# Performance work log

Hardware: AMD Instinct MI355X
Metric: run time of the kernel (lower is better)

## Reference

```python
import jax, jax.numpy as jnp
import numpy as np

B, Q, K, G, M = 16, 2048, 1024, 512, 4096
PC_MIN = np.array([-75.2, -75.2, -2.0], np.float32)
PC_MAX = np.array([75.2, 75.2, 4.0], np.float32)
MAX_SIZE = np.array([20.0, 20.0, 8.0], np.float32)


def decode_boxes(b):
    # normalized (cx,cy,cz,l,w,h,rad) in [0,1] -> metric (x,y,z,dx,dy,dz,heading)
    xyz = b[:, :3] * jnp.asarray(PC_MAX - PC_MIN) + jnp.asarray(PC_MIN)
    lwh = b[:, 3:6] * jnp.asarray(MAX_SIZE) + 0.05
    rad = b[:, 6:7] * (2.0 * np.pi) - np.pi
    return jnp.concatenate([xyz, lwh, rad], -1)


def box_cxcyczlwh_to_xyxyxy(b):
    c, s = b[:, :3], b[:, 3:6]
    return jnp.concatenate([c - 0.5 * s, c + 0.5 * s], -1)


def generalized_box3d_iou(b1, b2):
    # full pairwise axis-aligned 3D GIoU, as in the original module
    vol1 = jnp.prod(b1[:, 3:] - b1[:, :3], -1)
    vol2 = jnp.prod(b2[:, 3:] - b2[:, :3], -1)
    lt = jnp.maximum(b1[:, None, :3], b2[None, :, :3])
    rb = jnp.minimum(b1[:, None, 3:], b2[None, :, 3:])
    inter = jnp.prod(jnp.clip(rb - lt, 0.0), -1)
    union = vol1[:, None] + vol2[None, :] - inter
    iou = inter / jnp.clip(union, 1e-7)
    ltc = jnp.minimum(b1[:, None, :3], b2[None, :, :3])
    rbc = jnp.maximum(b1[:, None, 3:], b2[None, :, 3:])
    volc = jnp.prod(jnp.clip(rbc - ltc, 0.0), -1)
    return iou - (volc - union) / jnp.clip(volc, 1e-7)


def _bev_corners(b):
    c, s = jnp.cos(b[:, 6]), jnp.sin(b[:, 6])
    hx, hy = b[:, 3] * 0.5, b[:, 4] * 0.5
    lx = jnp.stack([hx, hx, -hx, -hx], -1)  # (N,4)
    ly = jnp.stack([hy, -hy, -hy, hy], -1)
    gx = b[:, 0:1] + lx * c[:, None] - ly * s[:, None]
    gy = b[:, 1:2] + lx * s[:, None] + ly * c[:, None]
    return jnp.stack([gx, gy], -1)  # (N,4,2)


def _points_in_box(pts, b):  # pts (N,P,2)
    c, s = jnp.cos(b[:, 6:7]), jnp.sin(b[:, 6:7])
    dx = pts[..., 0] - b[:, 0:1]
    dy = pts[..., 1] - b[:, 1:2]
    qx = dx * c + dy * s
    qy = -dx * s + dy * c
    return (jnp.abs(qx) <= b[:, 3:4] * 0.5 + 1e-5) & (jnp.abs(qy) <= b[:, 4:5] * 0.5 + 1e-5)


def _cross(a, b):
    return a[..., 0] * b[..., 1] - a[..., 1] * b[..., 0]


def paired_boxes_iou3d(bA, bB):
    # paired rotated 3D IoU (OpenPCDet paired_boxes_iou3d_gpu semantics)
    N = bA.shape[0]
    ca, cb = _bev_corners(bA), _bev_corners(bB)
    a0, a1 = ca, jnp.roll(ca, -1, axis=1)
    e0, e1 = cb, jnp.roll(cb, -1, axis=1)
    da = (a1 - a0)[:, :, None, :]
    db = (e1 - e0)[:, None, :, :]
    dp = e0[:, None, :, :] - a0[:, :, None, :]
    den = _cross(da, db)  # (N,4,4)
    den_s = jnp.where(jnp.abs(den) > 1e-8, den, 1.0)
    t = _cross(dp, db) / den_s
    u = _cross(dp, da) / den_s
    ok = (jnp.abs(den) > 1e-8) & (t >= 0.0) & (t <= 1.0) & (u >= 0.0) & (u <= 1.0)
    ipts = a0[:, :, None, :] + t[..., None] * da  # (N,4,4,2)
    pts = jnp.concatenate([ca, cb, ipts.reshape(N, 16, 2)], 1)  # (N,24,2)
    mask = jnp.concatenate([_points_in_box(ca, bB), _points_in_box(cb, bA), ok.reshape(N, 16)], 1)
    w = mask.astype(pts.dtype)
    cnt = w.sum(-1)
    cen = (pts * w[..., None]).sum(1) / jnp.maximum(cnt, 1.0)[:, None]
    ang = jnp.arctan2(pts[..., 1] - cen[:, None, 1], pts[..., 0] - cen[:, None, 0])
    ang = jnp.where(mask, ang, 1e9)
    order = jnp.argsort(ang, axis=1)
    pts_s = jnp.take_along_axis(pts, order[..., None], 1)
    mask_s = jnp.take_along_axis(mask, order, 1)
    p0 = pts_s[:, 0]
    poly = jnp.where(mask_s[..., None], pts_s, p0[:, None, :])
    x, y = poly[..., 0], poly[..., 1]
    xn, yn = jnp.roll(x, -1, 1), jnp.roll(y, -1, 1)
    area = 0.5 * jnp.abs(jnp.sum(x * yn - xn * y, 1))
    inter_bev = jnp.where(cnt >= 3.0, area, 0.0)
    z_lo = jnp.maximum(bA[:, 2] - bA[:, 5] * 0.5, bB[:, 2] - bB[:, 5] * 0.5)
    z_hi = jnp.minimum(bA[:, 2] + bA[:, 5] * 0.5, bB[:, 2] + bB[:, 5] * 0.5)
    inter = inter_bev * jnp.clip(z_hi - z_lo, 0.0)
    v1 = jnp.prod(bA[:, 3:6], -1)
    v2 = jnp.prod(bB[:, 3:6], -1)
    return inter / jnp.clip(v1 + v2 - inter, 1e-7)


def setup_inputs() -> dict:
    key = jax.random.key(0)
    ks = jax.random.split(key, 6)
    pred_boxes = jax.random.uniform(ks[0], (B, Q, 7), jnp.float32)
    pred_ious = jax.random.uniform(ks[1], (B, Q, 1), jnp.float32)
    gt_boxes = jax.random.uniform(ks[2], (B, G, 7), jnp.float32)
    topk_indexes = jax.random.randint(ks[3], (B, K, 1), 0, Q)
    batch_idx = jnp.repeat(jnp.arange(B), M // B)
    src_idx = jax.random.randint(ks[4], (M,), 0, K)
    tgt_idx = jax.random.randint(ks[5], (M,), 0, G)
    return {"pred_boxes": pred_boxes, "pred_ious": pred_ious, "gt_boxes": gt_boxes,
            "topk_indexes": topk_indexes, "batch_idx": batch_idx, "src_idx": src_idx,
            "tgt_idx": tgt_idx, "num_boxes": M}


def reference(pred_boxes, pred_ious, gt_boxes, topk_indexes, batch_idx, src_idx, tgt_idx, num_boxes):
    Bn = pred_boxes.shape[0]
    topk = topk_indexes[..., 0]                       # (B,K)
    brange = jnp.arange(Bn)[:, None]
    pb = pred_boxes[brange, topk]                     # (B,K,7) gather
    pi = pred_ious[brange, topk]                      # (B,K,1)
    mp = pb[batch_idx, src_idx]                       # (M,7) matched preds
    mt = gt_boxes[batch_idx, tgt_idx]                 # (M,7) matched targets
    src_boxes, src_rads = mp[:, :6], mp[:, 6:]
    tgt_boxes, tgt_rads = mt[:, :6], mt[:, 6:]
    loss_bbox = jnp.abs(src_boxes - tgt_boxes).sum()
    loss_rad = jnp.abs(src_rads - tgt_rads).sum()
    giou = generalized_box3d_iou(box_cxcyczlwh_to_xyxyxy(src_boxes), box_cxcyczlwh_to_xyxyxy(tgt_boxes))
    gt_iou = jnp.diagonal(giou)                       # only the diagonal of the MxM matrix is used
    loss_giou = (1.0 - gt_iou).sum()
    pim = pi[batch_idx, src_idx]                      # (M,1)
    iou_t = paired_boxes_iou3d(decode_boxes(mp), decode_boxes(mt)) * 2.0 - 1.0
    iou_t = jax.lax.stop_gradient(iou_t)              # .detach() in original
    loss_iou = jnp.abs(pim - iou_t[:, None]).sum()
    nb = jnp.asarray(num_boxes, pred_boxes.dtype)
    # order: [loss_bbox, loss_giou, loss_rad, loss_iou]
    return jnp.stack([loss_bbox, loss_giou, loss_rad, loss_iou]) / nb
```

## Files before the change

kernel.cpp:

```cpp
#include <hip/hip_runtime.h>

#define B_ 16
#define Q_ 2048
#define K_ 1024
#define G_ 512
#define M_ 4096

__device__ __forceinline__ float bsum32(float v) {
#pragma unroll
  for (int o = 1; o < 32; o <<= 1) v += __shfl_xor(v, o, 64);
  return v;
}

__device__ __forceinline__ void corner_xy(float cx, float cy, float hx, float hy,
                                          float c, float s, int idx,
                                          float& x, float& y) {
  float sx = (idx < 2) ? 1.f : -1.f;
  float sy = (idx == 0 || idx == 3) ? 1.f : -1.f;
  float lx = sx * hx, ly = sy * hy;
  x = cx + lx * c - ly * s;
  y = cy + lx * s + ly * c;
}

__global__ __launch_bounds__(256, 4) void pair_loss_kernel(
    const float* __restrict__ pred_boxes, const float* __restrict__ pred_ious,
    const float* __restrict__ gt_boxes, const int* __restrict__ topk_indexes,
    const int* __restrict__ batch_idx, const int* __restrict__ src_idx,
    const int* __restrict__ tgt_idx, float* __restrict__ partials) {
  const int lane = threadIdx.x & 63;
  const int wid = threadIdx.x >> 6;
  const int i = blockIdx.x * 4 + wid;

  const int b = __builtin_amdgcn_readfirstlane(batch_idx[i]);
  const int s = __builtin_amdgcn_readfirstlane(src_idx[i]);
  const int t = __builtin_amdgcn_readfirstlane(tgt_idx[i]);
  const int tk = __builtin_amdgcn_readfirstlane(topk_indexes[b * K_ + s]);
  const float* mp = pred_boxes + ((size_t)b * Q_ + tk) * 7;
  const float* mt = gt_boxes + ((size_t)b * G_ + t) * 7;
  const float pim = pred_ious[b * Q_ + tk];
  float A[7], Bv[7];
#pragma unroll
  for (int j = 0; j < 7; ++j) { A[j] = mp[j]; Bv[j] = mt[j]; }

  float lb = 0.f;
#pragma unroll
  for (int j = 0; j < 6; ++j) lb += fabsf(A[j] - Bv[j]);
  float lr = fabsf(A[6] - Bv[6]);

  float lg;
  {
    float vol1 = 1.f, vol2 = 1.f, inter = 1.f, volc = 1.f;
#pragma unroll
    for (int j = 0; j < 3; ++j) {
      float l1 = A[j] - 0.5f * A[3 + j], r1 = A[j] + 0.5f * A[3 + j];
      float l2 = Bv[j] - 0.5f * Bv[3 + j], r2 = Bv[j] + 0.5f * Bv[3 + j];
      vol1 *= (r1 - l1);
      vol2 *= (r2 - l2);
      inter *= fmaxf(fminf(r1, r2) - fmaxf(l1, l2), 0.f);
      volc *= fmaxf(fmaxf(r1, r2) - fminf(l1, l2), 0.f);
    }
    float uni = vol1 + vol2 - inter;
    float iou = inter / fmaxf(uni, 1e-7f);
    lg = 1.f - (iou - (volc - uni) / fmaxf(volc, 1e-7f));
  }

  float ax = A[0] * 150.4f - 75.2f;
  float ay = A[1] * 150.4f - 75.2f;
  float az = A[2] * 6.0f - 2.0f;
  float al = A[3] * 20.0f + 0.05f;
  float aw = A[4] * 20.0f + 0.05f;
  float ah = A[5] * 8.0f + 0.05f;
  float arad = A[6] * 6.2831853071795862f - 3.1415926535897931f;
  float bx = Bv[0] * 150.4f - 75.2f;
  float by = Bv[1] * 150.4f - 75.2f;
  float bz = Bv[2] * 6.0f - 2.0f;
  float bl = Bv[3] * 20.0f + 0.05f;
  float bw = Bv[4] * 20.0f + 0.05f;
  float bh = Bv[5] * 8.0f + 0.05f;
  float brad = Bv[6] * 6.2831853071795862f - 3.1415926535897931f;

  float cA = cosf(arad), sA = sinf(arad);
  float cB = cosf(brad), sB = sinf(brad);
  float ahx = al * 0.5f, ahy = aw * 0.5f;
  float bhx = bl * 0.5f, bhy = bw * 0.5f;

  float pxv = 0.f, pyv = 0.f;
  bool m = false;
  if (lane < 8) {
    bool isA = lane < 4;
    int ci = lane & 3;
    float ocx = isA ? ax : bx, ocy = isA ? ay : by;
    float ohx = isA ? ahx : bhx, ohy = isA ? ahy : bhy;
    float oc = isA ? cA : cB, os = isA ? sA : sB;
    float tcx = isA ? bx : ax, tcy = isA ? by : ay;
    float tl = isA ? bl : al, tw = isA ? bw : aw;
    float tc = isA ? cB : cA, ts = isA ? sB : sA;
    corner_xy(ocx, ocy, ohx, ohy, oc, os, ci, pxv, pyv);
    float dx = pxv - tcx, dy = pyv - tcy;
    float qx = dx * tc + dy * ts;
    float qy = -dx * ts + dy * tc;
    m = (fabsf(qx) <= tl * 0.5f + 1e-5f) && (fabsf(qy) <= tw * 0.5f + 1e-5f);
  } else if (lane < 24) {
    int e = lane - 8;
    int j = e >> 2, k = e & 3;
    float a0x, a0y, a1x, a1y, e0x, e0y, e1x, e1y;
    corner_xy(ax, ay, ahx, ahy, cA, sA, j, a0x, a0y);
    corner_xy(ax, ay, ahx, ahy, cA, sA, (j + 1) & 3, a1x, a1y);
    corner_xy(bx, by, bhx, bhy, cB, sB, k, e0x, e0y);
    corner_xy(bx, by, bhx, bhy, cB, sB, (k + 1) & 3, e1x, e1y);
    float dax = a1x - a0x, day = a1y - a0y;
    float dbx = e1x - e0x, dby = e1y - e0y;
    float dpx = e0x - a0x, dpy = e0y - a0y;
    float den = dax * dby - day * dbx;
    bool dok = fabsf(den) > 1e-8f;
    float dens = dok ? den : 1.f;
    float tt = (dpx * dby - dpy * dbx) / dens;
    float uu = (dpx * day - dpy * dax) / dens;
    m = dok && (tt >= 0.f) && (tt <= 1.f) && (uu >= 0.f) && (uu <= 1.f);
    pxv = a0x + tt * dax;
    pyv = a0y + tt * day;
  }

  unsigned long long mb = __ballot(m);
  int cnt = __popcll(mb);
  float sx = bsum32(m ? pxv : 0.f);
  float sy = bsum32(m ? pyv : 0.f);
  float cd = fmaxf((float)cnt, 1.f);
  float cenx = sx / cd, ceny = sy / cd;

  float pdx = pxv - cenx, pdy = pyv - ceny;
  float ad = fabsf(pdx) + fabsf(pdy);
  float tq = pdy / ad;
  float pa = (pdx >= 0.f) ? tq : ((pdy >= 0.f) ? 2.f - tq : -2.f - tq);
  if (ad == 0.f) pa = 0.f;
  float ap = m ? pa : 1e9f;

  int r = 0;
#pragma unroll
  for (int q = 0; q < 24; ++q) {
    float aq = __shfl(ap, q, 64);
    r += (aq < ap || (aq == ap && q < lane)) ? 1 : 0;
  }
  if (lane >= 24) r = lane;

  float sxr = __int_as_float(__builtin_amdgcn_ds_permute(r << 2, __float_as_int(pxv)));
  float syr = __int_as_float(__builtin_amdgcn_ds_permute(r << 2, __float_as_int(pyv)));

  int nidx = ((lane + 1 == cnt) ? 0 : (lane + 1)) & 63;
  float nx = __int_as_float(__builtin_amdgcn_ds_bpermute(nidx << 2, __float_as_int(sxr)));
  float ny = __int_as_float(__builtin_amdgcn_ds_bpermute(nidx << 2, __float_as_int(syr)));
  float cr = (lane < cnt) ? (sxr * ny - nx * syr) : 0.f;
  float area2 = bsum32(cr);
  float area = 0.5f * fabsf(area2);
  float inter_bev = (cnt >= 3) ? area : 0.f;

  float zlo = fmaxf(az - ah * 0.5f, bz - bh * 0.5f);
  float zhi = fminf(az + ah * 0.5f, bz + bh * 0.5f);
  float inter3 = inter_bev * fmaxf(zhi - zlo, 0.f);
  float v1 = al * aw * ah, v2 = bl * bw * bh;
  float iou3 = inter3 / fmaxf(v1 + v2 - inter3, 1e-7f);
  float li = fabsf(pim - (iou3 * 2.f - 1.f));

  __shared__ float wpart[4][4];
  if (lane == 0) {
    wpart[wid][0] = lb;
    wpart[wid][1] = lg;
    wpart[wid][2] = lr;
    wpart[wid][3] = li;
  }
  __syncthreads();
  if (threadIdx.x == 0) {
    float4 o;
    o.x = wpart[0][0] + wpart[1][0] + wpart[2][0] + wpart[3][0];
    o.y = wpart[0][1] + wpart[1][1] + wpart[2][1] + wpart[3][1];
    o.z = wpart[0][2] + wpart[1][2] + wpart[2][2] + wpart[3][2];
    o.w = wpart[0][3] + wpart[1][3] + wpart[2][3] + wpart[3][3];
    ((float4*)partials)[blockIdx.x] = o;
  }
}

__global__ __launch_bounds__(256) void finalize_kernel(
    const float* __restrict__ partials, const int* __restrict__ nb_ptr,
    float* __restrict__ out) {
  const int tid = threadIdx.x;
  const int lane = tid & 63;
  const int wid = tid >> 6;
  float4 acc = make_float4(0.f, 0.f, 0.f, 0.f);
#pragma unroll
  for (int k = 0; k < 4; ++k) {
    float4 p = ((const float4*)partials)[tid + 256 * k];
    acc.x += p.x; acc.y += p.y; acc.z += p.z; acc.w += p.w;
  }
#pragma unroll
  for (int o = 1; o < 64; o <<= 1) {
    acc.x += __shfl_xor(acc.x, o, 64);
    acc.y += __shfl_xor(acc.y, o, 64);
    acc.z += __shfl_xor(acc.z, o, 64);
    acc.w += __shfl_xor(acc.w, o, 64);
  }
  __shared__ float wpart[4][4];
  if (lane == 0) {
    wpart[wid][0] = acc.x; wpart[wid][1] = acc.y;
    wpart[wid][2] = acc.z; wpart[wid][3] = acc.w;
  }
  __syncthreads();
  if (tid == 0) {
    float nb = (float)nb_ptr[0];
    out[0] = (wpart[0][0] + wpart[1][0] + wpart[2][0] + wpart[3][0]) / nb;
    out[1] = (wpart[0][1] + wpart[1][1] + wpart[2][1] + wpart[3][1]) / nb;
    out[2] = (wpart[0][2] + wpart[1][2] + wpart[2][2] + wpart[3][2]) / nb;
    out[3] = (wpart[0][3] + wpart[1][3] + wpart[2][3] + wpart[3][3]) / nb;
  }
}

extern "C" void kernel_launch(void* const* d_in, const int* in_sizes, int n_in,
                              void* d_out, int out_size, void* d_ws, size_t ws_size,
                              hipStream_t stream) {
  const float* pred_boxes = (const float*)d_in[0];
  const float* pred_ious  = (const float*)d_in[1];
  const float* gt_boxes   = (const float*)d_in[2];
  const int* topk         = (const int*)d_in[3];
  const int* bidx         = (const int*)d_in[4];
  const int* sidx         = (const int*)d_in[5];
  const int* tidx         = (const int*)d_in[6];
  const int* nb           = (const int*)d_in[7];
  float* partials = (float*)d_ws;

  pair_loss_kernel<<<dim3(M_ / 4), dim3(256), 0, stream>>>(
      pred_boxes, pred_ious, gt_boxes, topk, bidx, sidx, tidx, partials);
  finalize_kernel<<<dim3(1), dim3(256), 0, stream>>>(partials, nb, (float*)d_out);
}
```

Measured before the change: 12.67 us.

## Fuse finalize reduction into main kernel via per-block flags and last-block spin

Merges the two launches into one kernel. Blocks grow to 1024 threads (16 pairs per block, 256 blocks), and each block publishes its partial sums and sets a release flag. Block 0 spin-waits on all flags, then reduces the partials and writes the final losses. This removes a second kernel launch and its dependency gap. The cost is a spin wait and a reliance on the flags in the workspace starting at zero and on all blocks being co-resident.

New measurement: 17.99 us. 1.42x slower.

```diff
diff --git a/kernel.cpp b/kernel.cpp
--- a/kernel.cpp
+++ b/kernel.cpp
@@ -5,10 +5,17 @@
 #define K_ 1024
 #define G_ 512
 #define M_ 4096
+#define NBLK 256
 
 __device__ __forceinline__ float bsum32(float v) {
 #pragma unroll
   for (int o = 1; o < 32; o <<= 1) v += __shfl_xor(v, o, 64);
+  return v;
+}
+
+__device__ __forceinline__ float bsum64(float v) {
+#pragma unroll
+  for (int o = 1; o < 64; o <<= 1) v += __shfl_xor(v, o, 64);
   return v;
 }
 
@@ -22,14 +29,17 @@
   y = cy + lx * s + ly * c;
 }
 
-__global__ __launch_bounds__(256, 4) void pair_loss_kernel(
+__global__ __launch_bounds__(1024, 4) void fused_loss_kernel(
     const float* __restrict__ pred_boxes, const float* __restrict__ pred_ious,
     const float* __restrict__ gt_boxes, const int* __restrict__ topk_indexes,
     const int* __restrict__ batch_idx, const int* __restrict__ src_idx,
-    const int* __restrict__ tgt_idx, float* __restrict__ partials) {
-  const int lane = threadIdx.x & 63;
-  const int wid = threadIdx.x >> 6;
-  const int i = blockIdx.x * 4 + wid;
+    const int* __restrict__ tgt_idx, const int* __restrict__ nb_ptr,
+    float* __restrict__ out, float* __restrict__ partials, int* __restrict__ tags) {
+  const int tid = threadIdx.x;
+  const int lane = tid & 63;
+  const int wid = tid >> 6;
+  const int blk = blockIdx.x;
+  const int i = blk * 16 + wid;
 
   const int b = __builtin_amdgcn_readfirstlane(batch_idx[i]);
   const int s = __builtin_amdgcn_readfirstlane(src_idx[i]);
@@ -145,7 +155,6 @@
 
   float sxr = __int_as_float(__builtin_amdgcn_ds_permute(r << 2, __float_as_int(pxv)));
   float syr = __int_as_float(__builtin_amdgcn_ds_permute(r << 2, __float_as_int(pyv)));
-
   int nidx = ((lane + 1 == cnt) ? 0 : (lane + 1)) & 63;
   float nx = __int_as_float(__builtin_amdgcn_ds_bpermute(nidx << 2, __float_as_int(sxr)));
   float ny = __int_as_float(__builtin_amdgcn_ds_bpermute(nidx << 2, __float_as_int(syr)));
@@ -161,7 +170,7 @@
   float iou3 = inter3 / fmaxf(v1 + v2 - inter3, 1e-7f);
   float li = fabsf(pim - (iou3 * 2.f - 1.f));
 
-  __shared__ float wpart[4][4];
+  __shared__ float wpart[16][4];
   if (lane == 0) {
     wpart[wid][0] = lb;
     wpart[wid][1] = lg;
@@ -169,47 +178,47 @@
     wpart[wid][3] = li;
   }
   __syncthreads();
-  if (threadIdx.x == 0) {
-    float4 o;
-    o.x = wpart[0][0] + wpart[1][0] + wpart[2][0] + wpart[3][0];
-    o.y = wpart[0][1] + wpart[1][1] + wpart[2][1] + wpart[3][1];
-    o.z = wpart[0][2] + wpart[1][2] + wpart[2][2] + wpart[3][2];
-    o.w = wpart[0][3] + wpart[1][3] + wpart[2][3] + wpart[3][3];
-    ((float4*)partials)[blockIdx.x] = o;
-  }
-}
-
-__global__ __launch_bounds__(256) void finalize_kernel(
-    const float* __restrict__ partials, const int* __restrict__ nb_ptr,
-    float* __restrict__ out) {
-  const int tid = threadIdx.x;
-  const int lane = tid & 63;
-  const int wid = tid >> 6;
-  float4 acc = make_float4(0.f, 0.f, 0.f, 0.f);
-#pragma unroll
-  for (int k = 0; k < 4; ++k) {
-    float4 p = ((const float4*)partials)[tid + 256 * k];
-    acc.x += p.x; acc.y += p.y; acc.z += p.z; acc.w += p.w;
-  }
-#pragma unroll
-  for (int o = 1; o < 64; o <<= 1) {
-    acc.x += __shfl_xor(acc.x, o, 64);
-    acc.y += __shfl_xor(acc.y, o, 64);
-    acc.z += __shfl_xor(acc.z, o, 64);
-    acc.w += __shfl_xor(acc.w, o, 64);
-  }
-  __shared__ float wpart[4][4];
-  if (lane == 0) {
-    wpart[wid][0] = acc.x; wpart[wid][1] = acc.y;
-    wpart[wid][2] = acc.z; wpart[wid][3] = acc.w;
+  if (tid < 4) {
+    float sacc = 0.f;
+#pragma unroll
+    for (int w = 0; w < 16; ++w) sacc += wpart[w][tid];
+    partials[blk * 4 + tid] = sacc;
   }
   __syncthreads();
   if (tid == 0) {
-    float nb = (float)nb_ptr[0];
-    out[0] = (wpart[0][0] + wpart[1][0] + wpart[2][0] + wpart[3][0]) / nb;
-    out[1] = (wpart[0][1] + wpart[1][1] + wpart[2][1] + wpart[3][1]) / nb;
-    out[2] = (wpart[0][2] + wpart[1][2] + wpart[2][2] + wpart[3][2]) / nb;
-    out[3] = (wpart[0][3] + wpart[1][3] + wpart[2][3] + wpart[3][3]) / nb;
+    __threadfence();
+    __hip_atomic_store(&tags[blk], 1, __ATOMIC_RELEASE, __HIP_MEMORY_SCOPE_AGENT);
+  }
+
+  if (blk == 0) {
+    if (tid < NBLK) {
+      while (__hip_atomic_load(&tags[tid], __ATOMIC_ACQUIRE,
+                               __HIP_MEMORY_SCOPE_AGENT) != 1) {
+      }
+    }
+    __syncthreads();
+    float4 p = make_float4(0.f, 0.f, 0.f, 0.f);
+    if (tid < NBLK) p = ((const float4*)partials)[tid];
+    p.x = bsum64(p.x);
+    p.y = bsum64(p.y);
+    p.z = bsum64(p.z);
+    p.w = bsum64(p.w);
+    __shared__ float fin[4][4];
+    if (tid < NBLK && lane == 0) {
+      fin[wid][0] = p.x; fin[wid][1] = p.y;
+      fin[wid][2] = p.z; fin[wid][3] = p.w;
+    }
+    __syncthreads();
+    if (tid == 0) {
+      float nb = (float)nb_ptr[0];
+      out[0] = (fin[0][0] + fin[1][0] + fin[2][0] + fin[3][0]) / nb;
+      out[1] = (fin[0][1] + fin[1][1] + fin[2][1] + fin[3][1]) / nb;
+      out[2] = (fin[0][2] + fin[1][2] + fin[2][2] + fin[3][2]) / nb;
+      out[3] = (fin[0][3] + fin[1][3] + fin[2][3] + fin[3][3]) / nb;
+    }
+    if (tid < NBLK) {
+      __hip_atomic_store(&tags[tid], 0, __ATOMIC_RELAXED, __HIP_MEMORY_SCOPE_AGENT);
+    }
   }
 }
 
@@ -225,8 +234,9 @@
   const int* tidx         = (const int*)d_in[6];
   const int* nb           = (const int*)d_in[7];
   float* partials = (float*)d_ws;
-
-  pair_loss_kernel<<<dim3(M_ / 4), dim3(256), 0, stream>>>(
-      pred_boxes, pred_ious, gt_boxes, topk, bidx, sidx, tidx, partials);
-  finalize_kernel<<<dim3(1), dim3(256), 0, stream>>>(partials, nb, (float*)d_out);
-}
+  int* tags = (int*)((char*)d_ws + NBLK * 4 * sizeof(float));
+
+  fused_loss_kernel<<<dim3(NBLK), dim3(1024), 0, stream>>>(
+      pred_boxes, pred_ious, gt_boxes, topk, bidx, sidx, tidx, nb,
+      (float*)d_out, partials, tags);
+}
```
